# Optimization experiments

Hardware: AMD Instinct MI355X
Metric: run time of the kernel (lower is better)

Reference implementation:

```python
import jax, jax.numpy as jnp
import numpy as np

B = 2048          # number of local graphs
L = 63            # local_edge_num -> 64 nodes per graph
N = B * (L + 1)   # 131072 total nodes
F = 32            # num_features
E = 524288        # random edges
C = 64            # gat hidden dim
A = 16            # action_dim
NEG_SLOPE = 0.2


def _gat(x, src, dst, W, a_src, a_dst, b, heads, out):
    """PyG-style GATConv (concat=True): gather -> leaky-relu logits ->
    per-destination segment softmax -> weighted scatter-sum."""
    n = x.shape[0]
    h = (x @ W).reshape(n, heads, out)                  # [N,H,C]
    al_s = jnp.sum(h * a_src, axis=-1)                  # [N,H]
    al_d = jnp.sum(h * a_dst, axis=-1)                  # [N,H]
    e = jax.nn.leaky_relu(al_s[src] + al_d[dst], NEG_SLOPE)  # [E,H]
    m = jax.ops.segment_max(e, dst, num_segments=n)
    e = jnp.exp(e - m[dst])
    s = jax.ops.segment_sum(e, dst, num_segments=n)
    alpha = e / (s[dst] + 1e-16)                        # [E,H]
    msg = h[src] * alpha[:, :, None]                    # [E,H,C]  dominant traffic
    agg = jax.ops.segment_sum(msg, dst, num_segments=n)
    return agg.reshape(n, heads * out) + b


def setup_inputs() -> dict:
    key = jax.random.key(0)
    ks = jax.random.split(key, 24)
    node_features = jax.random.normal(ks[0], (N, F), dtype=jnp.float32)
    edge_index = jax.random.randint(ks[1], (2, E), 0, N, dtype=jnp.int32)

    def p(k, shape, scale=0.1):
        return jax.random.normal(k, shape, dtype=jnp.float32) * scale

    return {
        "node_features": node_features,
        "edge_index": edge_index,
        # gat1: F -> 64, heads=4
        "W1": p(ks[2], (F, 4 * C)), "a1s": p(ks[3], (4, C)), "a1d": p(ks[4], (4, C)), "b1": jnp.zeros((4 * C,), jnp.float32),
        # gat2: 256 -> 64, heads=1
        "W2": p(ks[5], (4 * C, C)), "a2s": p(ks[6], (1, C)), "a2d": p(ks[7], (1, C)), "b2": jnp.zeros((C,), jnp.float32),
        # gat3: 64 -> 64, heads=1
        "W3": p(ks[8], (C, C)), "a3s": p(ks[9], (1, C)), "a3d": p(ks[10], (1, C)), "b3": jnp.zeros((C,), jnp.float32),
        # actor MLP
        "fcW1": p(ks[11], (C * (L + 1), 64)), "fcb1": jnp.zeros((64,), jnp.float32),
        "fcW2": p(ks[12], (64, 32)), "fcb2": jnp.zeros((32,), jnp.float32),
        "fcW3": p(ks[13], (32, A)), "fcb3": jnp.zeros((A,), jnp.float32),
    }


def reference(node_features, edge_index,
              W1, a1s, a1d, b1, W2, a2s, a2d, b2, W3, a3s, a3d, b3,
              fcW1, fcb1, fcW2, fcb2, fcW3, fcb3):
    n = node_features.shape[0]
    loops = jnp.arange(n, dtype=edge_index.dtype)       # GATConv add_self_loops=True
    src = jnp.concatenate([edge_index[0], loops])
    dst = jnp.concatenate([edge_index[1], loops])

    x = jax.nn.relu(_gat(node_features, src, dst, W1, a1s, a1d, b1, 4, C))
    x = jax.nn.relu(_gat(x, src, dst, W2, a2s, a2d, b2, 1, C))
    x = jax.nn.relu(_gat(x, src, dst, W3, a3s, a3d, b3, 1, C))

    x_gat = x.reshape(-1, C * (L + 1))                  # [B, 64*(L+1)]
    h = jax.nn.relu(x_gat @ fcW1 + fcb1)
    h = jax.nn.relu(h @ fcW2 + fcb2)
    action_mean = jax.nn.softmax(h @ fcW3 + fcb3, axis=-1)  # [B, A]
    return action_mean
```

## Files before the change

kernel.cpp:

```cpp
#include <hip/hip_runtime.h>
#include <math.h>

#define NN 131072
#define FF 32
#define EE 524288
#define ET (EE + NN)
#define BB 2048
#define KSPLIT 32

__global__ void init_counts(int* counts) {
  int i = blockIdx.x * 256 + threadIdx.x;
  counts[i] = 1;
}

__global__ void count_edges(const int* __restrict__ ei, int* counts) {
  int e = blockIdx.x * 256 + threadIdx.x;
  atomicAdd(&counts[ei[EE + e]], 1);
}

__global__ void scan_block(const int* __restrict__ counts, int* offs, int* blksums) {
  __shared__ int sd[256];
  int t = threadIdx.x;
  int i = blockIdx.x * 256 + t;
  int v = counts[i];
  sd[t] = v;
  __syncthreads();
  for (int o = 1; o < 256; o <<= 1) {
    int x = (t >= o) ? sd[t - o] : 0;
    __syncthreads();
    sd[t] += x;
    __syncthreads();
  }
  offs[i] = sd[t] - v;
  if (t == 255) blksums[blockIdx.x] = sd[255];
}

__global__ void scan_sums(int* blksums) {
  __shared__ int sd[512];
  int t = threadIdx.x;
  int v = blksums[t];
  sd[t] = v;
  __syncthreads();
  for (int o = 1; o < 512; o <<= 1) {
    int x = (t >= o) ? sd[t - o] : 0;
    __syncthreads();
    sd[t] += x;
    __syncthreads();
  }
  blksums[t] = sd[t] - v;
}

__global__ void scan_add(int* offs, int* cursor, const int* __restrict__ blksums) {
  int i = blockIdx.x * 256 + threadIdx.x;
  int o = offs[i] + blksums[blockIdx.x];
  offs[i] = o;
  cursor[i] = o;
  if (i == 0) offs[NN] = ET;
}

__global__ void fill_csr(const int* __restrict__ ei, int* cursor,
                         int* esrc, int* edst) {
  int i = blockIdx.x * 256 + threadIdx.x;
  int s, d;
  if (i < EE) { s = ei[i]; d = ei[EE + i]; }
  else        { s = d = i - EE; }
  int pos = atomicAdd(&cursor[d], 1);
  esrc[pos] = s;
  edst[pos] = d;
}

__global__ void l1_avec(const float* __restrict__ W1, const float* __restrict__ a1s,
                        const float* __restrict__ a1d, float* __restrict__ wts,
                        float* __restrict__ wtd) {
  int t = threadIdx.x;
  int h = t >> 5, k = t & 31;
  float as = 0.f, ad = 0.f;
  #pragma unroll
  for (int c = 0; c < 64; ++c) {
    float w = W1[k * 256 + h * 64 + c];
    as += w * a1s[h * 64 + c];
    ad += w * a1d[h * 64 + c];
  }
  wts[t] = as;
  wtd[t] = ad;
}

__global__ __launch_bounds__(256) void l1_logits(
    const float* __restrict__ x, const float* __restrict__ wts,
    const float* __restrict__ wtd, float* __restrict__ als, float* __restrict__ ald) {
  __shared__ float sx[64 * 33];
  __shared__ float sts[128], std_[128];
  int t = threadIdx.x;
  int n0 = blockIdx.x * 64;
  #pragma unroll
  for (int j = 0; j < 8; ++j) {
    int idx = t + j * 256;
    sx[(idx >> 5) * 33 + (idx & 31)] = x[(size_t)n0 * 32 + idx];
  }
  if (t < 128) sts[t] = wts[t]; else std_[t - 128] = wtd[t - 128];
  __syncthreads();
  int nl = t >> 2, h = t & 3;
  float vs = 0.f, vd = 0.f;
  #pragma unroll
  for (int k = 0; k < 32; ++k) {
    float xv = sx[nl * 33 + k];
    vs += xv * sts[h * 32 + k];
    vd += xv * std_[h * 32 + k];
  }
  als[(n0 + nl) * 4 + h] = vs;
  ald[(n0 + nl) * 4 + h] = vd;
}

__global__ void edge_w4(const int* __restrict__ esrc, const int* __restrict__ edst,
                        const float* __restrict__ als, const float* __restrict__ ald,
                        float4* __restrict__ w4) {
  int j = blockIdx.x * 256 + threadIdx.x;
  int s = esrc[j], d = edst[j];
  float4 a = ((const float4*)als)[s];
  float4 b = ((const float4*)ald)[d];
  float e0 = a.x + b.x; e0 = (e0 > 0.f) ? e0 : 0.2f * e0;
  float e1 = a.y + b.y; e1 = (e1 > 0.f) ? e1 : 0.2f * e1;
  float e2 = a.z + b.z; e2 = (e2 > 0.f) ? e2 : 0.2f * e2;
  float e3 = a.w + b.w; e3 = (e3 > 0.f) ? e3 : 0.2f * e3;
  w4[j] = make_float4(__expf(e0), __expf(e1), __expf(e2), __expf(e3));
}

__global__ void edge_w1(const int* __restrict__ esrc, const int* __restrict__ edst,
                        const float* __restrict__ als, const float* __restrict__ ald,
                        float* __restrict__ w) {
  int j = blockIdx.x * 256 + threadIdx.x;
  float e = als[esrc[j]] + ald[edst[j]];
  e = (e > 0.f) ? e : 0.2f * e;
  w[j] = __expf(e);
}

__global__ __launch_bounds__(256) void gat1_agg(
    const float* __restrict__ x, const int* __restrict__ offs,
    const int* __restrict__ esrc, const float4* __restrict__ w4arr,
    float* __restrict__ ya) {
  int t = threadIdx.x;
  int wv = t >> 6, lane = t & 63;
  int k = lane & 31, jp = lane >> 5;
  int n = blockIdx.x * 4 + wv;
  int start = offs[n], end = offs[n + 1];
  float xa0 = 0.f, xa1 = 0.f, xa2 = 0.f, xa3 = 0.f;
  float S0 = 0.f, S1 = 0.f, S2 = 0.f, S3 = 0.f;
  int j = start + jp;
  for (; j + 2 < end; j += 4) {
    int sA_ = esrc[j], sB_ = esrc[j + 2];
    float4 wA = w4arr[j], wB = w4arr[j + 2];
    float xA = x[(size_t)sA_ * 32 + k];
    float xB = x[(size_t)sB_ * 32 + k];
    xa0 += wA.x * xA; xa1 += wA.y * xA; xa2 += wA.z * xA; xa3 += wA.w * xA;
    S0 += wA.x; S1 += wA.y; S2 += wA.z; S3 += wA.w;
    xa0 += wB.x * xB; xa1 += wB.y * xB; xa2 += wB.z * xB; xa3 += wB.w * xB;
    S0 += wB.x; S1 += wB.y; S2 += wB.z; S3 += wB.w;
  }
  if (j < end) {
    int s = esrc[j];
    float4 w = w4arr[j];
    float xv = x[(size_t)s * 32 + k];
    xa0 += w.x * xv; xa1 += w.y * xv; xa2 += w.z * xv; xa3 += w.w * xv;
    S0 += w.x; S1 += w.y; S2 += w.z; S3 += w.w;
  }
  xa0 += __shfl_xor(xa0, 32); S0 += __shfl_xor(S0, 32);
  xa1 += __shfl_xor(xa1, 32); S1 += __shfl_xor(S1, 32);
  xa2 += __shfl_xor(xa2, 32); S2 += __shfl_xor(S2, 32);
  xa3 += __shfl_xor(xa3, 32); S3 += __shfl_xor(S3, 32);
  if (jp == 0) {
    ya[(size_t)n * 128 +  0 + k] = xa0 / (S0 + 1e-16f);
    ya[(size_t)n * 128 + 32 + k] = xa1 / (S1 + 1e-16f);
  } else {
    ya[(size_t)n * 128 + 64 + k] = xa2 / (S2 + 1e-16f);
    ya[(size_t)n * 128 + 96 + k] = xa3 / (S3 + 1e-16f);
  }
}

__global__ __launch_bounds__(256) void gemm1_bd(
    const float* __restrict__ ya, const float* __restrict__ W1,
    const float* __restrict__ b1, float* __restrict__ agg1) {
  __shared__ float sW1[32 * 256];
  __shared__ float sA[32 * 144];
  int t = threadIdx.x;
  int row0 = blockIdx.x * 32;
  #pragma unroll
  for (int j = 0; j < 8; ++j) {
    int li4 = t + j * 256;
    *(float4*)&sW1[li4 * 4] = *(const float4*)&W1[li4 * 4];
  }
  #pragma unroll
  for (int j = 0; j < 4; ++j) {
    int li = t + j * 256;
    int r = li >> 5, f4 = li & 31;
    int hh = f4 >> 3, kk4 = (f4 & 7) * 4;
    *(float4*)&sA[r * 144 + hh * 36 + kk4] =
        *(const float4*)&ya[(size_t)(row0 + r) * 128 + f4 * 4];
  }
  __syncthreads();
  int cq = t & 63;
  int rs = t >> 6;
  int hh = cq >> 4;
  float4 acc[8];
  #pragma unroll
  for (int rp = 0; rp < 8; ++rp) acc[rp] = make_float4(0.f, 0.f, 0.f, 0.f);
  #pragma unroll
  for (int kk = 0; kk < 32; ++kk) {
    float4 w4 = *(const float4*)&sW1[kk * 256 + cq * 4];
    #pragma unroll
    for (int rp = 0; rp < 8; ++rp) {
      float a = sA[(rs * 8 + rp) * 144 + hh * 36 + kk];
      acc[rp].x += a * w4.x; acc[rp].y += a * w4.y;
      acc[rp].z += a * w4.z; acc[rp].w += a * w4.w;
    }
  }
  float4 b4 = *(const float4*)&b1[cq * 4];
  #pragma unroll
  for (int rp = 0; rp < 8; ++rp) {
    int r = row0 + rs * 8 + rp;
    float4 v = acc[rp];
    v.x = fmaxf(v.x + b4.x, 0.f); v.y = fmaxf(v.y + b4.y, 0.f);
    v.z = fmaxf(v.z + b4.z, 0.f); v.w = fmaxf(v.w + b4.w, 0.f);
    *(float4*)&agg1[(size_t)r * 256 + cq * 4] = v;
  }
}

template <int KTILES, int ROWS, bool AL>
__global__ __launch_bounds__(256) void gemm_n64(
    const float* __restrict__ A, const float* __restrict__ W,
    const float* __restrict__ bias, const float* __restrict__ a_s,
    const float* __restrict__ a_d, float* __restrict__ out,
    float* __restrict__ als, float* __restrict__ ald) {
  constexpr int K = KTILES * 64;
  constexpr int RPT = ROWS / 16;
  constexpr int SAS = 68;
  __shared__ float sW[64 * 64];
  __shared__ float sA[ROWS * SAS];
  int t = threadIdx.x;
  int cq = t & 15;
  int rs = t >> 4;
  int row0 = blockIdx.x * ROWS;
  float4 acc[RPT];
  #pragma unroll
  for (int rp = 0; rp < RPT; ++rp) acc[rp] = make_float4(0.f, 0.f, 0.f, 0.f);
  for (int kt = 0; kt < KTILES; ++kt) {
    #pragma unroll
    for (int j = 0; j < 4; ++j) {
      int li = t + j * 256;
      int kk = li >> 4, cc = (li & 15) * 4;
      *(float4*)&sW[kk * 64 + cc] =
          *(const float4*)&W[(size_t)(kt * 64 + kk) * 64 + cc];
    }
    #pragma unroll
    for (int j = 0; j < ROWS / 16; ++j) {
      int li = t + j * 256;
      int r = li >> 4, kkq = (li & 15) * 4;
      *(float4*)&sA[r * SAS + kkq] =
          *(const float4*)&A[(size_t)(row0 + r) * K + kt * 64 + kkq];
    }
    __syncthreads();
    #pragma unroll
    for (int kq = 0; kq < 16; ++kq) {
      float4 a4[RPT];
      #pragma unroll
      for (int rp = 0; rp < RPT; ++rp)
        a4[rp] = *(const float4*)&sA[(rs * RPT + rp) * SAS + kq * 4];
      #pragma unroll
      for (int i = 0; i < 4; ++i) {
        float4 w4 = *(const float4*)&sW[(kq * 4 + i) * 64 + cq * 4];
        #pragma unroll
        for (int rp = 0; rp < RPT; ++rp) {
          float a = (i == 0) ? a4[rp].x : (i == 1) ? a4[rp].y
                  : (i == 2) ? a4[rp].z : a4[rp].w;
          acc[rp].x += a * w4.x; acc[rp].y += a * w4.y;
          acc[rp].z += a * w4.z; acc[rp].w += a * w4.w;
        }
      }
    }
    __syncthreads();
  }
  #pragma unroll
  for (int rp = 0; rp < RPT; ++rp) {
    int r = row0 + rs * RPT + rp;
    if constexpr (AL) {
      *(float4*)&out[(size_t)r * 64 + cq * 4] = acc[rp];
      float4 s4 = *(const float4*)&a_s[cq * 4];
      float4 d4 = *(const float4*)&a_d[cq * 4];
      float vs = acc[rp].x * s4.x + acc[rp].y * s4.y + acc[rp].z * s4.z + acc[rp].w * s4.w;
      float vd = acc[rp].x * d4.x + acc[rp].y * d4.y + acc[rp].z * d4.z + acc[rp].w * d4.w;
      #pragma unroll
      for (int o = 8; o >= 1; o >>= 1) { vs += __shfl_xor(vs, o); vd += __shfl_xor(vd, o); }
      if (cq == 0) { als[r] = vs; ald[r] = vd; }
    } else {
      float4 b4 = *(const float4*)&bias[cq * 4];
      float4 v = acc[rp];
      v.x = fmaxf(v.x + b4.x, 0.f); v.y = fmaxf(v.y + b4.y, 0.f);
      v.z = fmaxf(v.z + b4.z, 0.f); v.w = fmaxf(v.w + b4.w, 0.f);
      *(float4*)&out[(size_t)r * 64 + cq * 4] = v;
    }
  }
}

__global__ __launch_bounds__(256) void gemm_fc1_split(
    const float* __restrict__ A, const float* __restrict__ W,
    float* __restrict__ part) {
  __shared__ float sW[128 * 64];
  __shared__ float sA[16 * 132];
  int t = threadIdx.x;
  int bid = blockIdx.x;
  int rt = bid >> 5;
  int sp = bid & 31;
  #pragma unroll
  for (int j = 0; j < 8; ++j) {
    int li = t + j * 256;
    int kk = li >> 4, cc = (li & 15) * 4;
    *(float4*)&sW[kk * 64 + cc] =
        *(const float4*)&W[(size_t)(sp * 128 + kk) * 64 + cc];
  }
  #pragma unroll
  for (int j = 0; j < 2; ++j) {
    int li = t + j * 256;
    int r = li >> 5, kq4 = (li & 31) * 4;
    *(float4*)&sA[r * 132 + kq4] =
        *(const float4*)&A[(size_t)(rt * 16 + r) * 4096 + sp * 128 + kq4];
  }
  __syncthreads();
  int cq = t & 15;
  int rs = t >> 4;
  float4 acc = make_float4(0.f, 0.f, 0.f, 0.f);
  #pragma unroll
  for (int kq = 0; kq < 32; ++kq) {
    float4 a4 = *(const float4*)&sA[rs * 132 + kq * 4];
    #pragma unroll
    for (int i = 0; i < 4; ++i) {
      float4 w4 = *(const float4*)&sW[(kq * 4 + i) * 64 + cq * 4];
      float a = (i == 0) ? a4.x : (i == 1) ? a4.y : (i == 2) ? a4.z : a4.w;
      acc.x += a * w4.x; acc.y += a * w4.y; acc.z += a * w4.z; acc.w += a * w4.w;
    }
  }
  *(float4*)&part[((size_t)sp * BB + rt * 16 + rs) * 64 + cq * 4] = acc;
}

__global__ __launch_bounds__(256) void gat_aggregate(
    const float* __restrict__ hsrc, const float* __restrict__ warr,
    const int* __restrict__ offs, const int* __restrict__ esrc,
    const float* __restrict__ bias, float* __restrict__ out) {
  int wv = threadIdx.x >> 6;
  int lane = threadIdx.x & 63;
  int n = blockIdx.x * 4 + wv;
  int start = offs[n], end = offs[n + 1];
  float acc = 0.f, S = 0.f;
  int j = start;
  for (; j + 4 <= end; j += 4) {
    int s0 = esrc[j], s1 = esrc[j+1], s2 = esrc[j+2], s3 = esrc[j+3];
    float w0 = warr[j], w1 = warr[j+1], w2 = warr[j+2], w3 = warr[j+3];
    float v0 = hsrc[(size_t)s0 * 64 + lane];
    float v1 = hsrc[(size_t)s1 * 64 + lane];
    float v2 = hsrc[(size_t)s2 * 64 + lane];
    float v3 = hsrc[(size_t)s3 * 64 + lane];
    acc += w0 * v0; acc += w1 * v1; acc += w2 * v2; acc += w3 * v3;
    S += w0 + w1 + w2 + w3;
  }
  for (; j < end; ++j) {
    int s = esrc[j]; float w = warr[j];
    acc += w * hsrc[(size_t)s * 64 + lane];
    S += w;
  }
  float v = acc / (S + 1e-16f) + bias[lane];
  out[(size_t)n * 64 + lane] = fmaxf(v, 0.f);
}

__global__ __launch_bounds__(256) void fc23_softmax(
    const float* __restrict__ part, const float* __restrict__ fcb1,
    const float* __restrict__ W2, const float* __restrict__ b2,
    const float* __restrict__ W3, const float* __restrict__ b3,
    float* __restrict__ out) {
  int ws = threadIdx.x >> 6;
  int row = blockIdx.x * 4 + ws;
  int lane = threadIdx.x & 63;
  __shared__ float sh1[4][64];
  __shared__ float sh2[4][32];
  float h1 = fcb1[lane];
  #pragma unroll
  for (int sp = 0; sp < KSPLIT; sp += 4) {
    float p0 = part[((size_t)(sp + 0) * BB + row) * 64 + lane];
    float p1 = part[((size_t)(sp + 1) * BB + row) * 64 + lane];
    float p2 = part[((size_t)(sp + 2) * BB + row) * 64 + lane];
    float p3 = part[((size_t)(sp + 3) * BB + row) * 64 + lane];
    h1 += p0 + p1 + p2 + p3;
  }
  sh1[ws][lane] = fmaxf(h1, 0.f);
  if (lane < 32) {
    float acc = b2[lane];
    #pragma unroll
    for (int k = 0; k < 64; ++k) acc += sh1[ws][k] * W2[k * 32 + lane];
    sh2[ws][lane] = fmaxf(acc, 0.f);
  }
  float logit = -INFINITY;
  if (lane < 16) {
    float acc = b3[lane];
    #pragma unroll
    for (int k = 0; k < 32; ++k) acc += sh2[ws][k] * W3[k * 16 + lane];
    logit = acc;
  }
  float mx = logit;
  #pragma unroll
  for (int o = 8; o >= 1; o >>= 1) mx = fmaxf(mx, __shfl_xor(mx, o));
  float ex = (lane < 16) ? __expf(logit - mx) : 0.f;
  float ssum = ex;
  #pragma unroll
  for (int o = 8; o >= 1; o >>= 1) ssum += __shfl_xor(ssum, o);
  if (lane < 16) out[row * 16 + lane] = ex / ssum;
}

extern "C" void kernel_launch(void* const* d_in, const int* in_sizes, int n_in,
                              void* d_out, int out_size, void* d_ws, size_t ws_size,
                              hipStream_t stream) {
  const float* x0   = (const float*)d_in[0];
  const int*   ei   = (const int*)d_in[1];
  const float* W1   = (const float*)d_in[2];
  const float* a1s  = (const float*)d_in[3];
  const float* a1d  = (const float*)d_in[4];
  const float* b1   = (const float*)d_in[5];
  const float* W2   = (const float*)d_in[6];
  const float* a2s  = (const float*)d_in[7];
  const float* a2d  = (const float*)d_in[8];
  const float* b2   = (const float*)d_in[9];
  const float* W3   = (const float*)d_in[10];
  const float* a3s  = (const float*)d_in[11];
  const float* a3d  = (const float*)d_in[12];
  const float* b3   = (const float*)d_in[13];
  const float* fcW1 = (const float*)d_in[14];
  const float* fcb1 = (const float*)d_in[15];
  const float* fcW2 = (const float*)d_in[16];
  const float* fcb2 = (const float*)d_in[17];
  const float* fcW3 = (const float*)d_in[18];
  const float* fcb3 = (const float*)d_in[19];
  float* out = (float*)d_out;

  float* agg1   = (float*)d_ws;
  float* h23    = agg1 + (size_t)NN * 256;
  float* agg23  = h23 + (size_t)NN * 64;
  float* als1   = agg23 + (size_t)NN * 64;
  float* ald1   = als1 + (size_t)NN * 4;
  float* als2   = ald1 + (size_t)NN * 4;
  float* ald2   = als2 + NN;
  float* wts    = ald2 + NN;
  float* wtd    = wts + 128;
  int*   counts = (int*)(wtd + 128);
  int*   offs   = counts + NN;
  int*   cursor = offs + NN + 1;
  int*   esrc   = cursor + NN;
  int*   edst   = esrc + ET;
  int*   blksums= edst + ET;
  float4* w41   = (float4*)agg1;
  float* ya     = h23;
  float* als3   = agg1;
  float* ald3   = agg1 + NN;
  float* w2     = agg1 + 2 * (size_t)NN;
  float* w3arr  = w2 + ET;
  float* part   = w3arr + ET;

  init_counts<<<NN / 256, 256, 0, stream>>>(counts);
  count_edges<<<EE / 256, 256, 0, stream>>>(ei, counts);
  scan_block<<<NN / 256, 256, 0, stream>>>(counts, offs, blksums);
  scan_sums<<<1, 512, 0, stream>>>(blksums);
  scan_add<<<NN / 256, 256, 0, stream>>>(offs, cursor, blksums);
  fill_csr<<<ET / 256, 256, 0, stream>>>(ei, cursor, esrc, edst);

  l1_avec<<<1, 128, 0, stream>>>(W1, a1s, a1d, wts, wtd);
  l1_logits<<<NN / 64, 256, 0, stream>>>(x0, wts, wtd, als1, ald1);
  edge_w4<<<ET / 256, 256, 0, stream>>>(esrc, edst, als1, ald1, w41);
  gat1_agg<<<NN / 4, 256, 0, stream>>>(x0, offs, esrc, w41, ya);
  gemm1_bd<<<NN / 32, 256, 0, stream>>>(ya, W1, b1, agg1);
  gemm_n64<4, 32, true><<<NN / 32, 256, 0, stream>>>(agg1, W2, nullptr, a2s, a2d, h23, als2, ald2);
  edge_w1<<<ET / 256, 256, 0, stream>>>(esrc, edst, als2, ald2, w2);
  gat_aggregate<<<NN / 4, 256, 0, stream>>>(h23, w2, offs, esrc, b2, agg23);
  gemm_n64<1, 32, true><<<NN / 32, 256, 0, stream>>>(agg23, W3, nullptr, a3s, a3d, h23, als3, ald3);
  edge_w1<<<ET / 256, 256, 0, stream>>>(esrc, edst, als3, ald3, w3arr);
  gat_aggregate<<<NN / 4, 256, 0, stream>>>(h23, w3arr, offs, esrc, b3, agg23);
  gemm_fc1_split<<<128 * KSPLIT, 256, 0, stream>>>(agg23, fcW1, part);
  fc23_softmax<<<BB / 4, 256, 0, stream>>>(part, fcb1, fcW2, fcb2, fcW3, fcb3, out);
}
```

Before: 514.2 us.

## Fuse layer-1 block-diagonal GEMM with layer-2 GEMM and logits in one kernel

```diff
diff --git a/kernel.cpp b/kernel.cpp
--- a/kernel.cpp
+++ b/kernel.cpp
@@ -176,51 +176,106 @@
   }
 }
 
-__global__ __launch_bounds__(256) void gemm1_bd(
+__global__ __launch_bounds__(256) void gat2_fused(
     const float* __restrict__ ya, const float* __restrict__ W1,
-    const float* __restrict__ b1, float* __restrict__ agg1) {
-  __shared__ float sW1[32 * 256];
-  __shared__ float sA[32 * 144];
-  int t = threadIdx.x;
-  int row0 = blockIdx.x * 32;
-  #pragma unroll
-  for (int j = 0; j < 8; ++j) {
-    int li4 = t + j * 256;
-    *(float4*)&sW1[li4 * 4] = *(const float4*)&W1[li4 * 4];
-  }
-  #pragma unroll
-  for (int j = 0; j < 4; ++j) {
-    int li = t + j * 256;
-    int r = li >> 5, f4 = li & 31;
-    int hh = f4 >> 3, kk4 = (f4 & 7) * 4;
-    *(float4*)&sA[r * 144 + hh * 36 + kk4] =
-        *(const float4*)&ya[(size_t)(row0 + r) * 128 + f4 * 4];
-  }
-  __syncthreads();
-  int cq = t & 63;
-  int rs = t >> 6;
-  int hh = cq >> 4;
-  float4 acc[8];
-  #pragma unroll
-  for (int rp = 0; rp < 8; ++rp) acc[rp] = make_float4(0.f, 0.f, 0.f, 0.f);
-  #pragma unroll
-  for (int kk = 0; kk < 32; ++kk) {
-    float4 w4 = *(const float4*)&sW1[kk * 256 + cq * 4];
-    #pragma unroll
-    for (int rp = 0; rp < 8; ++rp) {
-      float a = sA[(rs * 8 + rp) * 144 + hh * 36 + kk];
-      acc[rp].x += a * w4.x; acc[rp].y += a * w4.y;
-      acc[rp].z += a * w4.z; acc[rp].w += a * w4.w;
-    }
-  }
-  float4 b4 = *(const float4*)&b1[cq * 4];
-  #pragma unroll
-  for (int rp = 0; rp < 8; ++rp) {
-    int r = row0 + rs * 8 + rp;
-    float4 v = acc[rp];
-    v.x = fmaxf(v.x + b4.x, 0.f); v.y = fmaxf(v.y + b4.y, 0.f);
-    v.z = fmaxf(v.z + b4.z, 0.f); v.w = fmaxf(v.w + b4.w, 0.f);
-    *(float4*)&agg1[(size_t)r * 256 + cq * 4] = v;
+    const float* __restrict__ b1, const float* __restrict__ W2,
+    const float* __restrict__ a_s, const float* __restrict__ a_d,
+    float* __restrict__ h2, float* __restrict__ als, float* __restrict__ ald) {
+  __shared__ float sYa[64 * 36];
+  __shared__ float sT1[64 * 68];
+  __shared__ float sW1c[32 * 64];
+  __shared__ float sW2[64 * 64];
+  int t = threadIdx.x;
+  int row0 = blockIdx.x * 64;
+  int cq = t & 15;
+  int rs = t >> 4;
+  float4 acc2[4];
+  #pragma unroll
+  for (int rp = 0; rp < 4; ++rp) acc2[rp] = make_float4(0.f, 0.f, 0.f, 0.f);
+  for (int kt = 0; kt < 4; ++kt) {
+    if (kt > 0) __syncthreads();
+    #pragma unroll
+    for (int j = 0; j < 2; ++j) {
+      int li = t + j * 256;
+      int r = li >> 3, f4i = li & 7;
+      *(float4*)&sYa[r * 36 + f4i * 4] =
+          *(const float4*)&ya[(size_t)(row0 + r) * 128 + kt * 32 + f4i * 4];
+    }
+    #pragma unroll
+    for (int j = 0; j < 2; ++j) {
+      int li = t + j * 256;
+      int kk = li >> 4, cc = (li & 15) * 4;
+      *(float4*)&sW1c[kk * 64 + cc] =
+          *(const float4*)&W1[(size_t)kk * 256 + kt * 64 + cc];
+    }
+    #pragma unroll
+    for (int j = 0; j < 4; ++j) {
+      int li = t + j * 256;
+      int kk = li >> 4, cc = (li & 15) * 4;
+      *(float4*)&sW2[kk * 64 + cc] =
+          *(const float4*)&W2[(size_t)(kt * 64 + kk) * 64 + cc];
+    }
+    __syncthreads();
+    float4 acc1[4];
+    #pragma unroll
+    for (int rp = 0; rp < 4; ++rp) acc1[rp] = make_float4(0.f, 0.f, 0.f, 0.f);
+    #pragma unroll
+    for (int kq = 0; kq < 8; ++kq) {
+      float4 a4[4];
+      #pragma unroll
+      for (int rp = 0; rp < 4; ++rp)
+        a4[rp] = *(const float4*)&sYa[(rs * 4 + rp) * 36 + kq * 4];
+      #pragma unroll
+      for (int i = 0; i < 4; ++i) {
+        float4 w4 = *(const float4*)&sW1c[(kq * 4 + i) * 64 + cq * 4];
+        #pragma unroll
+        for (int rp = 0; rp < 4; ++rp) {
+          float a = (i == 0) ? a4[rp].x : (i == 1) ? a4[rp].y
+                  : (i == 2) ? a4[rp].z : a4[rp].w;
+          acc1[rp].x += a * w4.x; acc1[rp].y += a * w4.y;
+          acc1[rp].z += a * w4.z; acc1[rp].w += a * w4.w;
+        }
+      }
+    }
+    float4 b4 = *(const float4*)&b1[kt * 64 + cq * 4];
+    #pragma unroll
+    for (int rp = 0; rp < 4; ++rp) {
+      float4 v = acc1[rp];
+      v.x = fmaxf(v.x + b4.x, 0.f); v.y = fmaxf(v.y + b4.y, 0.f);
+      v.z = fmaxf(v.z + b4.z, 0.f); v.w = fmaxf(v.w + b4.w, 0.f);
+      *(float4*)&sT1[(rs * 4 + rp) * 68 + cq * 4] = v;
+    }
+    __syncthreads();
+    #pragma unroll
+    for (int kq = 0; kq < 16; ++kq) {
+      float4 a4[4];
+      #pragma unroll
+      for (int rp = 0; rp < 4; ++rp)
+        a4[rp] = *(const float4*)&sT1[(rs * 4 + rp) * 68 + kq * 4];
+      #pragma unroll
+      for (int i = 0; i < 4; ++i) {
+        float4 w4 = *(const float4*)&sW2[(kq * 4 + i) * 64 + cq * 4];
+        #pragma unroll
+        for (int rp = 0; rp < 4; ++rp) {
+          float a = (i == 0) ? a4[rp].x : (i == 1) ? a4[rp].y
+                  : (i == 2) ? a4[rp].z : a4[rp].w;
+          acc2[rp].x += a * w4.x; acc2[rp].y += a * w4.y;
+          acc2[rp].z += a * w4.z; acc2[rp].w += a * w4.w;
+        }
+      }
+    }
+  }
+  float4 s4 = *(const float4*)&a_s[cq * 4];
+  float4 d4 = *(const float4*)&a_d[cq * 4];
+  #pragma unroll
+  for (int rp = 0; rp < 4; ++rp) {
+    int r = row0 + rs * 4 + rp;
+    *(float4*)&h2[(size_t)r * 64 + cq * 4] = acc2[rp];
+    float vs = acc2[rp].x * s4.x + acc2[rp].y * s4.y + acc2[rp].z * s4.z + acc2[rp].w * s4.w;
+    float vd = acc2[rp].x * d4.x + acc2[rp].y * d4.y + acc2[rp].z * d4.z + acc2[rp].w * d4.w;
+    #pragma unroll
+    for (int o = 8; o >= 1; o >>= 1) { vs += __shfl_xor(vs, o); vd += __shfl_xor(vd, o); }
+    if (cq == 0) { als[r] = vs; ald[r] = vd; }
   }
 }
 
@@ -453,12 +508,13 @@
   int*   edst   = esrc + ET;
   int*   blksums= edst + ET;
   float4* w41   = (float4*)agg1;
+  float* h2     = agg1 + ((size_t)4 << 20);
+  float* als3   = agg1 + ((size_t)13 << 20);
+  float* ald3   = als3 + NN;
+  float* w2     = agg1 + ((size_t)14 << 20);
+  float* w3arr  = w2 + ET;
+  float* part   = agg1 + ((size_t)16 << 20);
   float* ya     = h23;
-  float* als3   = agg1;
-  float* ald3   = agg1 + NN;
-  float* w2     = agg1 + 2 * (size_t)NN;
-  float* w3arr  = w2 + ET;
-  float* part   = w3arr + ET;
 
   init_counts<<<NN / 256, 256, 0, stream>>>(counts);
   count_edges<<<EE / 256, 256, 0, stream>>>(ei, counts);
@@ -471,11 +527,10 @@
   l1_logits<<<NN / 64, 256, 0, stream>>>(x0, wts, wtd, als1, ald1);
   edge_w4<<<ET / 256, 256, 0, stream>>>(esrc, edst, als1, ald1, w41);
   gat1_agg<<<NN / 4, 256, 0, stream>>>(x0, offs, esrc, w41, ya);
-  gemm1_bd<<<NN / 32, 256, 0, stream>>>(ya, W1, b1, agg1);
-  gemm_n64<4, 32, true><<<NN / 32, 256, 0, stream>>>(agg1, W2, nullptr, a2s, a2d, h23, als2, ald2);
+  gat2_fused<<<NN / 64, 256, 0, stream>>>(ya, W1, b1, W2, a2s, a2d, h2, als2, ald2);
   edge_w1<<<ET / 256, 256, 0, stream>>>(esrc, edst, als2, ald2, w2);
-  gat_aggregate<<<NN / 4, 256, 0, stream>>>(h23, w2, offs, esrc, b2, agg23);
-  gemm_n64<1, 32, true><<<NN / 32, 256, 0, stream>>>(agg23, W3, nullptr, a3s, a3d, h23, als3, ald3);
+  gat_aggregate<<<NN / 4, 256, 0, stream>>>(h2, w2, offs, esrc, b2, agg23);
+  gemm_n64<1, 64, true><<<NN / 64, 256, 0, stream>>>(agg23, W3, nullptr, a3s, a3d, h23, als3, ald3);
   edge_w1<<<ET / 256, 256, 0, stream>>>(esrc, edst, als3, ald3, w3arr);
   gat_aggregate<<<NN / 4, 256, 0, stream>>>(h23, w3arr, offs, esrc, b3, agg23);
   gemm_fc1_split<<<128 * KSPLIT, 256, 0, stream>>>(agg23, fcW1, part);
```

New measurement: 498.8 us. -3.0%, faster.
